# Performance work log

Measured on AMD Instinct MI355X. Metric: run time of the kernel, lower is better.

## Reference

```python
import jax, jax.numpy as jnp
import numpy as np

NUM_HEADS = 8
HEAD_DIM = 128
MAX_RES = 224.0


def rope_embed(feat_shape, dim, max_res=MAX_RES):
    # timm pixel_freq_bands: 2**linspace(0, log2(max_res)-1, dim//4) * pi
    num_bands = dim // 4
    bands = (2.0 ** jnp.linspace(0.0, float(np.log2(max_res)) - 1.0, num_bands)) * jnp.pi
    # pixel coords in [-1, 1] per spatial dim
    coords = [jnp.linspace(-1.0, 1.0, s) for s in feat_shape]
    grid = jnp.stack(jnp.meshgrid(*coords, indexing='ij'), axis=-1)[..., None]  # [H,W,2,1]
    pos = grid * bands  # [H,W,2,num_bands]
    n = int(np.prod(feat_shape))
    sin = jnp.repeat(jnp.sin(pos).reshape(n, -1), 2, axis=-1)  # [n, dim]
    cos = jnp.repeat(jnp.cos(pos).reshape(n, -1), 2, axis=-1)  # [n, dim]
    return sin, cos


def _rot(x):
    # interleaved rotate-half: (x0,x1,x2,x3,...) -> (-x1,x0,-x3,x2,...)
    return jnp.stack([-x[..., 1::2], x[..., ::2]], axis=-1).reshape(x.shape)


def setup_inputs() -> dict:
    key = jax.random.key(0)
    k1, k2, k3, k4 = jax.random.split(key, 4)
    C, E = 1024, 1024
    x = jax.random.normal(k1, (64, C, 16, 16), dtype=jnp.float32)
    qkv_w = jax.random.normal(k2, (3 * E, C), dtype=jnp.float32) * (C ** -0.5)
    qkv_b = jnp.zeros((3 * E,), dtype=jnp.float32)
    proj_w = jax.random.normal(k3, (E, E), dtype=jnp.float32) * (E ** -0.5)
    proj_b = jax.random.normal(k4, (E,), dtype=jnp.float32) * 0.02
    return {"x": x, "qkv_w": qkv_w, "qkv_b": qkv_b, "proj_w": proj_w, "proj_b": proj_b}


def reference(x, qkv_w, qkv_b, proj_w, proj_b):
    B, C, H, W = x.shape
    n = H * W
    scale = HEAD_DIM ** -0.5
    sin_emb, cos_emb = rope_embed((H, W), HEAD_DIM)  # [n, head_dim]

    t = x.reshape(B, C, n).transpose(0, 2, 1)                      # [B, n, C]
    t = jnp.concatenate([t.mean(axis=1, keepdims=True), t], axis=1)  # [B, n+1, C]

    qkv = t @ qkv_w.T + qkv_b                                      # [B, n+1, 3E]
    qkv = qkv.reshape(B, n + 1, 3, NUM_HEADS, HEAD_DIM).transpose(2, 0, 3, 1, 4)
    q, k, v = qkv[0], qkv[1], qkv[2]                               # [B, h, n+1, d]

    def apply_rope(z):
        zc, zs = z[:, :, :1], z[:, :, 1:]
        zs = zs * cos_emb + _rot(zs) * sin_emb
        return jnp.concatenate([zc, zs], axis=2)

    q = apply_rope(q)
    k = apply_rope(k)

    attn = jax.nn.softmax(jnp.einsum('bhqd,bhkd->bhqk', q, k) * scale, axis=-1)
    out = jnp.einsum('bhqk,bhkd->bhqd', attn, v)
    out = out.transpose(0, 2, 1, 3).reshape(B, n + 1, -1)           # [B, n+1, E]
    out = out @ proj_w.T + proj_b
    return out[:, 0]
```

## Files before the change

### kernel.cpp

```cpp
#include <hip/hip_runtime.h>
#include <math.h>

#define PI_F 3.14159265358979323846f
#define KSTEP 0.21959209425992272f

using bf16x8 = __attribute__((ext_vector_type(8))) short;
using f32x4 = __attribute__((ext_vector_type(4))) float;
using u16x8 = __attribute__((ext_vector_type(8))) unsigned short;

static __device__ __forceinline__ float wave_reduce_sum(float v) {
#pragma unroll
  for (int off = 32; off; off >>= 1) v += __shfl_down(v, off);
  return v;
}

static __device__ __forceinline__ unsigned short f2bf(float f) {
  unsigned u = __float_as_uint(f);
  return (unsigned short)((u + 0x7fffu + ((u >> 16) & 1u)) >> 16);
}

static __device__ __forceinline__ float bf2f(unsigned short s) {
  return __uint_as_float(((unsigned)s) << 16);
}

static __device__ __forceinline__ void gload_lds16(const void* g, void* l) {
  __builtin_amdgcn_global_load_lds((const __attribute__((address_space(1))) unsigned int*)g,
                                   (__attribute__((address_space(3))) unsigned int*)l, 16, 0, 0);
}

__global__ __launch_bounds__(256) void prep_kernel(const float* __restrict__ x,
                                                   const float* __restrict__ qkv_w,
                                                   unsigned short* __restrict__ xt,
                                                   float* __restrict__ t_mean,
                                                   unsigned short* __restrict__ wk_bf,
                                                   float2* __restrict__ sc) {
  const int bid = blockIdx.x;
  const int t = threadIdx.x;
  __shared__ float tile[64][33];
  if (bid < 1024) {
    const int ct = bid & 15, b = bid >> 4;
    const int cl = t >> 2, pq = (t & 3) * 8;
    const int pl = t >> 3, cq = (t & 7) * 8;
    float sum = 0.0f;
    const float* xrow = x + ((size_t)(b * 1024 + ct * 64 + cl) * 256) + pq;
    unsigned short* xtb = xt + (size_t)b * 262144 + ct * 64;
    for (int pt = 0; pt < 8; ++pt) {
      const float4 v0 = *reinterpret_cast<const float4*>(xrow + pt * 32);
      const float4 v1 = *reinterpret_cast<const float4*>(xrow + pt * 32 + 4);
      tile[cl][pq + 0] = v0.x; tile[cl][pq + 1] = v0.y; tile[cl][pq + 2] = v0.z; tile[cl][pq + 3] = v0.w;
      tile[cl][pq + 4] = v1.x; tile[cl][pq + 5] = v1.y; tile[cl][pq + 6] = v1.z; tile[cl][pq + 7] = v1.w;
      sum += (v0.x + v0.y) + (v0.z + v0.w) + (v1.x + v1.y) + (v1.z + v1.w);
      __syncthreads();
      u16x8 o;
#pragma unroll
      for (int e = 0; e < 8; ++e) o[e] = f2bf(tile[cq + e][pl]);
      *reinterpret_cast<u16x8*>(xtb + (size_t)(pt * 32 + pl) * 1024 + cq) = o;
      __syncthreads();
    }
    sum += __shfl_xor(sum, 1);
    sum += __shfl_xor(sum, 2);
    if ((t & 3) == 0) t_mean[b * 1024 + ct * 64 + cl] = sum * (1.0f / 256.0f);
  } else if (bid < 2048) {
    const int i = ((bid - 1024) * 256 + t) * 4;
    const float4 v = *reinterpret_cast<const float4*>(qkv_w + 1048576 + i);
    ushort4 r;
    r.x = f2bf(v.x); r.y = f2bf(v.y); r.z = f2bf(v.z); r.w = f2bf(v.w);
    *reinterpret_cast<ushort4*>(wk_bf + i) = r;
  } else {
    const int idx = (bid - 2048) * 256 + t;
    const int m = idx >> 8, j = idx & 255;
    const float band = exp2f((float)(m & 31) * KSTEP) * PI_F;
    const float coord = (m < 32) ? (-1.0f + (2.0f / 15.0f) * (float)(j >> 4))
                                 : (-1.0f + (2.0f / 15.0f) * (float)(j & 15));
    float sn, cs;
    sincosf(coord * band, &sn, &cs);
    sc[idx] = make_float2(sn, cs);
  }
}

__global__ __launch_bounds__(256) void gemm_splitk(
    const float* __restrict__ A, int lda, int aStrideZ,
    const float* __restrict__ B, int ldb, int bStrideZ,
    float* __restrict__ Cp, int ldc, int cStrideZ, int cStrideKc, int KC) {
  const int nt = blockIdx.x, mt = blockIdx.y;
  const int z = blockIdx.z / KC, kc = blockIdx.z % KC;
  const int tid = threadIdx.x;
  A += (size_t)z * aStrideZ + (size_t)mt * 32 * lda + kc * 256;
  B += (size_t)z * bStrideZ + (size_t)nt * 64 * ldb + kc * 256;
  Cp += (size_t)kc * cStrideKc + (size_t)z * cStrideZ + (size_t)mt * 32 * ldc + nt * 64;

  __shared__ float As[32][34];
  __shared__ float Bs[32][68];

  const int tm = tid >> 4;
  const int tn = tid & 15;
  float acc0[4] = {0, 0, 0, 0}, acc1[4] = {0, 0, 0, 0};

  for (int k0 = 0; k0 < 256; k0 += 32) {
    {
      const int m = tid >> 3, kq = tid & 7;
      float4 v = *reinterpret_cast<const float4*>(A + (size_t)m * lda + k0 + kq * 4);
      As[kq * 4 + 0][m] = v.x; As[kq * 4 + 1][m] = v.y;
      As[kq * 4 + 2][m] = v.z; As[kq * 4 + 3][m] = v.w;
    }
#pragma unroll
    for (int r = 0; r < 2; ++r) {
      const int idx = r * 256 + tid;
      const int n = idx >> 3, kq = idx & 7;
      float4 v = *reinterpret_cast<const float4*>(B + (size_t)n * ldb + k0 + kq * 4);
      Bs[kq * 4 + 0][n] = v.x; Bs[kq * 4 + 1][n] = v.y;
      Bs[kq * 4 + 2][n] = v.z; Bs[kq * 4 + 3][n] = v.w;
    }
    __syncthreads();
#pragma unroll
    for (int k = 0; k < 32; ++k) {
      const float a0 = As[k][tm * 2], a1 = As[k][tm * 2 + 1];
      const float4 bb = *reinterpret_cast<const float4*>(&Bs[k][tn * 4]);
      acc0[0] += a0 * bb.x; acc0[1] += a0 * bb.y; acc0[2] += a0 * bb.z; acc0[3] += a0 * bb.w;
      acc1[0] += a1 * bb.x; acc1[1] += a1 * bb.y; acc1[2] += a1 * bb.z; acc1[3] += a1 * bb.w;
    }
    __syncthreads();
  }
  *reinterpret_cast<float4*>(Cp + (size_t)(tm * 2) * ldc + tn * 4) =
      make_float4(acc0[0], acc0[1], acc0[2], acc0[3]);
  *reinterpret_cast<float4*>(Cp + (size_t)(tm * 2 + 1) * ldc + tn * 4) =
      make_float4(acc1[0], acc1[1], acc1[2], acc1[3]);
}

__global__ __launch_bounds__(256) void gemm_proj_splitk(
    const float* __restrict__ Apart, const float* __restrict__ abias,
    const float* __restrict__ B, float* __restrict__ Cp) {
  const int nt = blockIdx.x, mt = blockIdx.y, kc = blockIdx.z;
  const int tid = threadIdx.x;
  B += (size_t)nt * 64 * 1024 + kc * 256;
  Cp += (size_t)kc * 65536 + (size_t)mt * 32 * 1024 + nt * 64;

  __shared__ float As[32][34];
  __shared__ float Bs[32][68];

  const int tm = tid >> 4;
  const int tn = tid & 15;
  float acc0[4] = {0, 0, 0, 0}, acc1[4] = {0, 0, 0, 0};

  for (int k0 = 0; k0 < 256; k0 += 32) {
    {
      const int m = tid >> 3, kq = tid & 7;
      const int kg = kc * 256 + k0 + kq * 4;
      const float* Ab = Apart + (size_t)(mt * 32 + m) * 1024 + kg;
      float4 v = *reinterpret_cast<const float4*>(abias + kg);
#pragma unroll
      for (int r = 0; r < 4; ++r) {
        const float4 p = *reinterpret_cast<const float4*>(Ab + (size_t)r * 65536);
        v.x += p.x; v.y += p.y; v.z += p.z; v.w += p.w;
      }
      As[kq * 4 + 0][m] = v.x; As[kq * 4 + 1][m] = v.y;
      As[kq * 4 + 2][m] = v.z; As[kq * 4 + 3][m] = v.w;
    }
#pragma unroll
    for (int r = 0; r < 2; ++r) {
      const int idx = r * 256 + tid;
      const int n = idx >> 3, kq = idx & 7;
      float4 v = *reinterpret_cast<const float4*>(B + (size_t)n * 1024 + k0 + kq * 4);
      Bs[kq * 4 + 0][n] = v.x; Bs[kq * 4 + 1][n] = v.y;
      Bs[kq * 4 + 2][n] = v.z; Bs[kq * 4 + 3][n] = v.w;
    }
    __syncthreads();
#pragma unroll
    for (int k = 0; k < 32; ++k) {
      const float a0 = As[k][tm * 2], a1 = As[k][tm * 2 + 1];
      const float4 bb = *reinterpret_cast<const float4*>(&Bs[k][tn * 4]);
      acc0[0] += a0 * bb.x; acc0[1] += a0 * bb.y; acc0[2] += a0 * bb.z; acc0[3] += a0 * bb.w;
      acc1[0] += a1 * bb.x; acc1[1] += a1 * bb.y; acc1[2] += a1 * bb.z; acc1[3] += a1 * bb.w;
    }
    __syncthreads();
  }
  *reinterpret_cast<float4*>(Cp + (size_t)(tm * 2) * 1024 + tn * 4) =
      make_float4(acc0[0], acc0[1], acc0[2], acc0[3]);
  *reinterpret_cast<float4*>(Cp + (size_t)(tm * 2 + 1) * 1024 + tn * 4) =
      make_float4(acc1[0], acc1[1], acc1[2], acc1[3]);
}

__global__ __launch_bounds__(256) void reduce4_bias(const float* __restrict__ part,
                                                    const float* __restrict__ bias,
                                                    float* __restrict__ out) {
  const int i = blockIdx.x * 256 + threadIdx.x;
  out[i] = part[i] + part[i + 65536] + part[i + 131072] + part[i + 196608] + bias[i & 1023];
}

__global__ __launch_bounds__(512, 1) void k_scores_mfma(
    const unsigned short* __restrict__ wk, const unsigned short* __restrict__ xt,
    const float* __restrict__ qkv_b, const float* __restrict__ q0p,
    const float2* __restrict__ sc, float* __restrict__ attn) {
  const int l = blockIdx.x;
  const int b = ((l >> 5) << 3) | (l & 7);
  const int mt = (l >> 3) & 3;
  const int tid = threadIdx.x;
  const int w = tid >> 6, lane = tid & 63;
  const int wr = w >> 2, wc = w & 3;

  __shared__ __align__(16) char smem[131072];

  const unsigned short* wkA = wk + (size_t)(mt * 256) * 1024;
  const unsigned short* xtb = xt + (size_t)b * 262144;

  f32x4 acc[8][4] = {};

#define STAGE4(tt, src)                                                          \
  {                                                                              \
    char* base_ = smem + ((tt)&3) * 32768;                                       \
    const int c0_ = (src)*32;                                                    \
    _Pragma("unroll") for (int c = 0; c < 2; ++c) {                              \
      const int rb_ = w * 2 + c;                                                 \
      const int row_ = rb_ * 16 + (lane >> 2);                                   \
      const int sl_ = ((lane & 3) ^ ((row_ >> 1) & 3)) * 8;                      \
      gload_lds16(wkA + (size_t)row_ * 1024 + c0_ + sl_, base_ + rb_ * 1024);    \
      gload_lds16(xtb + (size_t)row_ * 1024 + c0_ + sl_,                         \
                  base_ + 16384 + rb_ * 1024);                                   \
    }                                                                            \
  }

  STAGE4(0, 0);
  STAGE4(1, 1);
  STAGE4(2, 2);

  for (int t = 0; t < 32; ++t) {
    {
      const int tt = t + 3;
      const int src = tt > 31 ? 31 : tt;
      STAGE4(tt, src);
    }
    asm volatile("s_waitcnt vmcnt(12)" ::: "memory");
    __builtin_amdgcn_s_barrier();
    const char* Ab = smem + (t & 3) * 32768;
    const char* Bb = Ab + 16384;
    bf16x8 bfrag[4];
#pragma unroll
    for (int ni = 0; ni < 4; ++ni) {
      const int row = wc * 64 + ni * 16 + (lane & 15);
      bfrag[ni] = *reinterpret_cast<const bf16x8*>(
          Bb + row * 64 + (((lane >> 4) ^ ((row >> 1) & 3)) << 4));
    }
#pragma unroll
    for (int mh = 0; mh < 2; ++mh) {
      bf16x8 af[4];
#pragma unroll
      for (int q = 0; q < 4; ++q) {
        const int row = wr * 128 + (mh * 4 + q) * 16 + (lane & 15);
        af[q] = *reinterpret_cast<const bf16x8*>(
            Ab + row * 64 + (((lane >> 4) ^ ((row >> 1) & 3)) << 4));
      }
      __builtin_amdgcn_s_setprio(1);
#pragma unroll
      for (int q = 0; q < 4; ++q)
#pragma unroll
        for (int ni = 0; ni < 4; ++ni)
          acc[mh * 4 + q][ni] = __builtin_amdgcn_mfma_f32_16x16x32_bf16(
              af[q], bfrag[ni], acc[mh * 4 + q][ni], 0, 0, 0);
      __builtin_amdgcn_s_setprio(0);
    }
    __builtin_amdgcn_s_barrier();
    asm volatile("" ::: "memory");
  }
#undef STAGE4

  asm volatile("s_waitcnt vmcnt(0)" ::: "memory");
  __syncthreads();

  float* q0_lds = reinterpret_cast<float*>(smem);
  float* k0_lds = q0_lds + 256;
  float* Sh = k0_lds + 256;
  float* ps = Sh + 520;
  float* r4 = ps + 4;

  if (tid < 256) {
    const float* qp = q0p + (size_t)b * 2048 + mt * 256 + tid;
    q0_lds[tid] = qkv_b[mt * 256 + tid] + qp[0] + qp[131072] + qp[262144] + qp[393216];
    const float* kp = qp + 1024;
    k0_lds[tid] = qkv_b[1024 + mt * 256 + tid] + kp[0] + kp[131072] + kp[262144] + kp[393216];
  }
  __syncthreads();

  if (tid < 256) {
    float pr = q0_lds[tid] * k0_lds[tid];
    pr = wave_reduce_sum(pr);
    if (lane == 0) ps[tid >> 6] = pr;
  }

  const int colj = lane & 15, rgrp = lane >> 4;
  const float* bk = qkv_b + 1024 + mt * 256 + wr * 128;
  float partial[4] = {0, 0, 0, 0};
#pragma unroll
  for (int mi = 0; mi < 8; ++mi) {
#pragma unroll
    for (int pp = 0; pp < 2; ++pp) {
      const int dd = mi * 16 + rgrp * 4 + pp * 2;
      const int m = dd >> 1;
      const float2 qv = *reinterpret_cast<const float2*>(q0_lds + wr * 128 + dd);
      const float2 bv = *reinterpret_cast<const float2*>(bk + dd);
#pragma unroll
      for (int ni = 0; ni < 4; ++ni) {
        const int j = wc * 64 + ni * 16 + colj;
        const float ke = acc[mi][ni][pp * 2] + bv.x;
        const float ko = acc[mi][ni][pp * 2 + 1] + bv.y;
        const float2 tt = sc[m * 256 + j];
        partial[ni] += tt.y * (ke * qv.x + ko * qv.y) + tt.x * (ke * qv.y - ko * qv.x);
      }
    }
  }
#pragma unroll
  for (int ni = 0; ni < 4; ++ni) {
    partial[ni] += __shfl_xor(partial[ni], 16);
    partial[ni] += __shfl_xor(partial[ni], 32);
  }
  if (lane < 16) {
#pragma unroll
    for (int ni = 0; ni < 4; ++ni)
      Sh[wr * 260 + 1 + wc * 64 + ni * 16 + colj] = partial[ni];
  }
  __syncthreads();
  if (tid == 0) { Sh[0] = ps[0] + ps[1]; Sh[260] = ps[2] + ps[3]; }
  __syncthreads();

  const int hg = tid >> 8, i = tid & 255;
  const float scale = 0.08838834764831845f;
  const float* Sr = Sh + hg * 260;
  const float va = Sr[i] * scale;
  const float vb = (i == 0) ? Sr[256] * scale : -3.0e38f;
  float mx = fmaxf(va, vb);
#pragma unroll
  for (int off = 32; off; off >>= 1) mx = fmaxf(mx, __shfl_xor(mx, off));
  if (lane == 0) r4[hg * 4 + ((tid >> 6) & 3)] = mx;
  __syncthreads();
  mx = fmaxf(fmaxf(r4[hg * 4], r4[hg * 4 + 1]), fmaxf(r4[hg * 4 + 2], r4[hg * 4 + 3]));
  const float ea = expf(va - mx);
  const float eb = (i == 0) ? expf(vb - mx) : 0.0f;
  float sum = ea + eb;
#pragma unroll
  for (int off = 32; off; off >>= 1) sum += __shfl_xor(sum, off);
  __syncthreads();
  if (lane == 0) r4[hg * 4 + ((tid >> 6) & 3)] = sum;
  __syncthreads();
  sum = r4[hg * 4] + r4[hg * 4 + 1] + r4[hg * 4 + 2] + r4[hg * 4 + 3];
  const float inv = 1.0f / sum;
  float* ab = attn + (size_t)(b * 8 + 2 * mt + hg) * 257;
  ab[i] = ea * inv;
  if (i == 0) ab[256] = eb * inv;
}

__global__ __launch_bounds__(256) void u_accum_kernel(const unsigned short* __restrict__ xt,
                                                      const float* __restrict__ t_mean,
                                                      const float* __restrict__ attn,
                                                      float* __restrict__ u) {
  const int ct = blockIdx.x;
  const int b = blockIdx.y;
  const int tid = threadIdx.x;
  __shared__ float aw[2056];
  __shared__ float red[8192];
  for (int i = tid; i < 2056; i += 256) aw[i] = attn[(size_t)(b * 8 + (i & 7)) * 257 + (i >> 3)];
  __syncthreads();
  const int cl = tid & 31, q = tid >> 5;
  const int c = ct * 128 + cl * 4;
  const unsigned short* xr = xt + (size_t)b * 262144 + c;
  float acc[8][4] = {};
  for (int p = q * 32; p < q * 32 + 32; ++p) {
    const ushort4 v = *reinterpret_cast<const ushort4*>(xr + (size_t)p * 1024);
    const float xs[4] = {bf2f(v.x), bf2f(v.y), bf2f(v.z), bf2f(v.w)};
    const float* w8 = &aw[(p + 1) * 8];
#pragma unroll
    for (int hh = 0; hh < 8; ++hh)
#pragma unroll
      for (int e = 0; e < 4; ++e) acc[hh][e] += w8[hh] * xs[e];
  }
#pragma unroll
  for (int hh = 0; hh < 8; ++hh)
#pragma unroll
    for (int e = 0; e < 4; ++e) red[q * 1024 + (cl * 8 + hh) * 4 + e] = acc[hh][e];
  __syncthreads();
#pragma unroll
  for (int r = 0; r < 4; ++r) {
    const int o = tid * 4 + r;
    const int cl2 = o >> 5, hh = (o >> 2) & 7, e = o & 3;
    float s = 0.0f;
#pragma unroll
    for (int qq = 0; qq < 8; ++qq) s += red[qq * 1024 + o];
    const int cc = ct * 128 + cl2 * 4 + e;
    s += aw[hh] * t_mean[b * 1024 + cc];
    u[(size_t)(b * 8 + hh) * 1024 + cc] = s;
  }
}

extern "C" void kernel_launch(void* const* d_in, const int* in_sizes, int n_in,
                              void* d_out, int out_size, void* d_ws, size_t ws_size,
                              hipStream_t stream) {
  const float* x = (const float*)d_in[0];
  const float* qkv_w = (const float*)d_in[1];
  const float* qkv_b = (const float*)d_in[2];
  const float* proj_w = (const float*)d_in[3];
  const float* proj_b = (const float*)d_in[4];
  float* out = (float*)d_out;

  float* ws = (float*)d_ws;
  float* t_mean = ws;
  float* q0k0_part = ws + 65536;
  float* attn = ws + 721408;
  float* u = ws + 852992;
  float* out0_part = ws + 1377280;
  float* out_part = ws + 1639424;
  float2* sc = (float2*)(ws + 1901568);
  unsigned short* wk_bf = (unsigned short*)(ws + 1934336);
  unsigned short* x_t = (unsigned short*)(ws + 2458624);

  prep_kernel<<<2112, 256, 0, stream>>>(x, qkv_w, x_t, t_mean, wk_bf, sc);

  gemm_splitk<<<dim3(32, 2, 4), 256, 0, stream>>>(t_mean, 1024, 0, qkv_w, 1024, 0,
                                                  q0k0_part, 2048, 0, 131072, 4);

  k_scores_mfma<<<256, 512, 0, stream>>>(wk_bf, x_t, qkv_b, q0k0_part, sc, attn);

  u_accum_kernel<<<dim3(8, 64), 256, 0, stream>>>(x_t, t_mean, attn, u);

  gemm_splitk<<<dim3(2, 2, 32), 256, 0, stream>>>(u, 8192, 1024,
                                                  qkv_w + (size_t)2048 * 1024, 1024, 131072,
                                                  out0_part, 1024, 128, 65536, 4);

  gemm_proj_splitk<<<dim3(16, 2, 4), 256, 0, stream>>>(out0_part, qkv_b + 2048, proj_w, out_part);

  reduce4_bias<<<256, 256, 0, stream>>>(out_part, proj_b, out);
}
```

Baseline: 110.1 us.

## Retile scores kernel per head and fuse value projection into u accumulation

The scores kernel now gives each block one head (128 rows) instead of two, halving the accumulators. It switches from a 4-stage to a 3-stage LDS ring with a smaller footprint and raises launch bounds so more blocks can be resident, and the grid doubles to 512 blocks. The u accumulation kernel now also multiplies the per-head u slice by the V weights directly from LDS, writing 8 split-K partials. This removes the separate u buffer and one split-K GEMM launch, and the proj GEMM's A-reduction grows from 4 to 8 partials. The risk is that fp32 weight reads inside the fused kernel are less efficient than the dedicated GEMM.

```diff
diff --git a/kernel.cpp b/kernel.cpp
--- a/kernel.cpp
+++ b/kernel.cpp
@@ -149,7 +149,7 @@
       const float* Ab = Apart + (size_t)(mt * 32 + m) * 1024 + kg;
       float4 v = *reinterpret_cast<const float4*>(abias + kg);
 #pragma unroll
-      for (int r = 0; r < 4; ++r) {
+      for (int r = 0; r < 8; ++r) {
         const float4 p = *reinterpret_cast<const float4*>(Ab + (size_t)r * 65536);
         v.x += p.x; v.y += p.y; v.z += p.z; v.w += p.w;
       }
@@ -187,115 +187,115 @@
   out[i] = part[i] + part[i + 65536] + part[i + 131072] + part[i + 196608] + bias[i & 1023];
 }
 
-__global__ __launch_bounds__(512, 1) void k_scores_mfma(
+__global__ __launch_bounds__(512, 4) void k_scores_mfma(
     const unsigned short* __restrict__ wk, const unsigned short* __restrict__ xt,
     const float* __restrict__ qkv_b, const float* __restrict__ q0p,
     const float2* __restrict__ sc, float* __restrict__ attn) {
   const int l = blockIdx.x;
-  const int b = ((l >> 5) << 3) | (l & 7);
-  const int mt = (l >> 3) & 3;
+  const int b = ((l >> 6) << 3) | (l & 7);
+  const int h = (l >> 3) & 7;
   const int tid = threadIdx.x;
   const int w = tid >> 6, lane = tid & 63;
   const int wr = w >> 2, wc = w & 3;
 
-  __shared__ __align__(16) char smem[131072];
-
-  const unsigned short* wkA = wk + (size_t)(mt * 256) * 1024;
+  __shared__ __align__(16) char smem[73728];
+
+  const unsigned short* wkh = wk + (size_t)h * 131072;
   const unsigned short* xtb = xt + (size_t)b * 262144;
 
-  f32x4 acc[8][4] = {};
-
-#define STAGE4(tt, src)                                                          \
-  {                                                                              \
-    char* base_ = smem + ((tt)&3) * 32768;                                       \
-    const int c0_ = (src)*32;                                                    \
-    _Pragma("unroll") for (int c = 0; c < 2; ++c) {                              \
-      const int rb_ = w * 2 + c;                                                 \
-      const int row_ = rb_ * 16 + (lane >> 2);                                   \
-      const int sl_ = ((lane & 3) ^ ((row_ >> 1) & 3)) * 8;                      \
-      gload_lds16(wkA + (size_t)row_ * 1024 + c0_ + sl_, base_ + rb_ * 1024);    \
-      gload_lds16(xtb + (size_t)row_ * 1024 + c0_ + sl_,                         \
-                  base_ + 16384 + rb_ * 1024);                                   \
-    }                                                                            \
-  }
-
-  STAGE4(0, 0);
-  STAGE4(1, 1);
-  STAGE4(2, 2);
-
+  f32x4 acc[4][4] = {};
+
+#define STAGE6(buf, c0)                                                     \
+  {                                                                         \
+    char* Ab_ = smem + (buf)*24576;                                         \
+    char* Bb_ = Ab_ + 8192;                                                 \
+    {                                                                       \
+      const int row_ = w * 16 + (lane >> 2);                                \
+      const int sl_ = ((lane & 3) ^ ((row_ >> 1) & 3)) * 8;                 \
+      gload_lds16(wkh + (size_t)row_ * 1024 + (c0) + sl_, Ab_ + w * 1024);  \
+    }                                                                       \
+    _Pragma("unroll") for (int i = 0; i < 2; ++i) {                         \
+      const int row_ = w * 32 + i * 16 + (lane >> 2);                       \
+      const int sl_ = ((lane & 3) ^ ((row_ >> 1) & 3)) * 8;                 \
+      gload_lds16(xtb + (size_t)row_ * 1024 + (c0) + sl_,                   \
+                  Bb_ + (w * 2 + i) * 1024);                                \
+    }                                                                       \
+  }
+
+  STAGE6(0, 0);
+  STAGE6(1, 32);
+  int cur = 0, nxt = 2;
   for (int t = 0; t < 32; ++t) {
     {
-      const int tt = t + 3;
-      const int src = tt > 31 ? 31 : tt;
-      STAGE4(tt, src);
-    }
-    asm volatile("s_waitcnt vmcnt(12)" ::: "memory");
+      const int src = (t + 2 > 31) ? 31 : (t + 2);
+      STAGE6(nxt, src * 32);
+    }
+    asm volatile("s_waitcnt vmcnt(6)" ::: "memory");
     __builtin_amdgcn_s_barrier();
-    const char* Ab = smem + (t & 3) * 32768;
-    const char* Bb = Ab + 16384;
-    bf16x8 bfrag[4];
+    const char* Ab = smem + cur * 24576;
+    const char* Bb = Ab + 8192;
+    bf16x8 af[4], bfr[4];
+#pragma unroll
+    for (int mi = 0; mi < 4; ++mi) {
+      const int row = wr * 64 + mi * 16 + (lane & 15);
+      af[mi] = *reinterpret_cast<const bf16x8*>(
+          Ab + row * 64 + (((lane >> 4) ^ ((row >> 1) & 3)) << 4));
+    }
 #pragma unroll
     for (int ni = 0; ni < 4; ++ni) {
       const int row = wc * 64 + ni * 16 + (lane & 15);
-      bfrag[ni] = *reinterpret_cast<const bf16x8*>(
+      bfr[ni] = *reinterpret_cast<const bf16x8*>(
           Bb + row * 64 + (((lane >> 4) ^ ((row >> 1) & 3)) << 4));
     }
-#pragma unroll
-    for (int mh = 0; mh < 2; ++mh) {
-      bf16x8 af[4];
-#pragma unroll
-      for (int q = 0; q < 4; ++q) {
-        const int row = wr * 128 + (mh * 4 + q) * 16 + (lane & 15);
-        af[q] = *reinterpret_cast<const bf16x8*>(
-            Ab + row * 64 + (((lane >> 4) ^ ((row >> 1) & 3)) << 4));
-      }
-      __builtin_amdgcn_s_setprio(1);
-#pragma unroll
-      for (int q = 0; q < 4; ++q)
-#pragma unroll
-        for (int ni = 0; ni < 4; ++ni)
-          acc[mh * 4 + q][ni] = __builtin_amdgcn_mfma_f32_16x16x32_bf16(
-              af[q], bfrag[ni], acc[mh * 4 + q][ni], 0, 0, 0);
-      __builtin_amdgcn_s_setprio(0);
-    }
+    __builtin_amdgcn_s_setprio(1);
+#pragma unroll
+    for (int mi = 0; mi < 4; ++mi)
+#pragma unroll
+      for (int ni = 0; ni < 4; ++ni)
+        acc[mi][ni] =
+            __builtin_amdgcn_mfma_f32_16x16x32_bf16(af[mi], bfr[ni], acc[mi][ni], 0, 0, 0);
+    __builtin_amdgcn_s_setprio(0);
     __builtin_amdgcn_s_barrier();
     asm volatile("" ::: "memory");
-  }
-#undef STAGE4
+    cur = (cur == 2) ? 0 : cur + 1;
+    nxt = (nxt == 2) ? 0 : nxt + 1;
+  }
+#undef STAGE6
 
   asm volatile("s_waitcnt vmcnt(0)" ::: "memory");
   __syncthreads();
 
   float* q0_lds = reinterpret_cast<float*>(smem);
-  float* k0_lds = q0_lds + 256;
-  float* Sh = k0_lds + 256;
-  float* ps = Sh + 520;
-  float* r4 = ps + 4;
-
-  if (tid < 256) {
-    const float* qp = q0p + (size_t)b * 2048 + mt * 256 + tid;
-    q0_lds[tid] = qkv_b[mt * 256 + tid] + qp[0] + qp[131072] + qp[262144] + qp[393216];
+  float* k0_lds = q0_lds + 128;
+  float* red2 = k0_lds + 128;
+  float* ps = red2 + 512;
+  float* r4a = ps + 2;
+  float* r4b = r4a + 4;
+
+  if (tid < 128) {
+    const float* qp = q0p + (size_t)b * 2048 + h * 128 + tid;
+    q0_lds[tid] = qkv_b[h * 128 + tid] + qp[0] + qp[131072] + qp[262144] + qp[393216];
     const float* kp = qp + 1024;
-    k0_lds[tid] = qkv_b[1024 + mt * 256 + tid] + kp[0] + kp[131072] + kp[262144] + kp[393216];
-  }
-  __syncthreads();
-
-  if (tid < 256) {
+    k0_lds[tid] = qkv_b[1024 + h * 128 + tid] + kp[0] + kp[131072] + kp[262144] + kp[393216];
+  }
+  __syncthreads();
+
+  if (tid < 128) {
     float pr = q0_lds[tid] * k0_lds[tid];
     pr = wave_reduce_sum(pr);
-    if (lane == 0) ps[tid >> 6] = pr;
+    if (lane == 0) ps[w] = pr;
   }
 
   const int colj = lane & 15, rgrp = lane >> 4;
-  const float* bk = qkv_b + 1024 + mt * 256 + wr * 128;
+  const float* bk = qkv_b + 1024 + h * 128;
   float partial[4] = {0, 0, 0, 0};
 #pragma unroll
-  for (int mi = 0; mi < 8; ++mi) {
+  for (int mi = 0; mi < 4; ++mi) {
 #pragma unroll
     for (int pp = 0; pp < 2; ++pp) {
-      const int dd = mi * 16 + rgrp * 4 + pp * 2;
+      const int dd = wr * 64 + mi * 16 + rgrp * 4 + pp * 2;
       const int m = dd >> 1;
-      const float2 qv = *reinterpret_cast<const float2*>(q0_lds + wr * 128 + dd);
+      const float2 qv = *reinterpret_cast<const float2*>(q0_lds + dd);
       const float2 bv = *reinterpret_cast<const float2*>(bk + dd);
 #pragma unroll
       for (int ni = 0; ni < 4; ++ni) {
@@ -314,48 +314,53 @@
   }
   if (lane < 16) {
 #pragma unroll
-    for (int ni = 0; ni < 4; ++ni)
-      Sh[wr * 260 + 1 + wc * 64 + ni * 16 + colj] = partial[ni];
-  }
-  __syncthreads();
-  if (tid == 0) { Sh[0] = ps[0] + ps[1]; Sh[260] = ps[2] + ps[3]; }
-  __syncthreads();
-
-  const int hg = tid >> 8, i = tid & 255;
+    for (int ni = 0; ni < 4; ++ni) red2[(wc * 64 + ni * 16 + colj) * 2 + wr] = partial[ni];
+  }
+  __syncthreads();
+
   const float scale = 0.08838834764831845f;
-  const float* Sr = Sh + hg * 260;
-  const float va = Sr[i] * scale;
-  const float vb = (i == 0) ? Sr[256] * scale : -3.0e38f;
+  float va = -3.0e38f, vb = -3.0e38f;
+  if (tid < 256) {
+    va = scale * ((tid == 0) ? (ps[0] + ps[1]) : (red2[(tid - 1) * 2] + red2[(tid - 1) * 2 + 1]));
+    if (tid == 0) vb = scale * (red2[255 * 2] + red2[255 * 2 + 1]);
+  }
   float mx = fmaxf(va, vb);
-#pragma unroll
-  for (int off = 32; off; off >>= 1) mx = fmaxf(mx, __shfl_xor(mx, off));
-  if (lane == 0) r4[hg * 4 + ((tid >> 6) & 3)] = mx;
-  __syncthreads();
-  mx = fmaxf(fmaxf(r4[hg * 4], r4[hg * 4 + 1]), fmaxf(r4[hg * 4 + 2], r4[hg * 4 + 3]));
-  const float ea = expf(va - mx);
-  const float eb = (i == 0) ? expf(vb - mx) : 0.0f;
-  float sum = ea + eb;
-#pragma unroll
-  for (int off = 32; off; off >>= 1) sum += __shfl_xor(sum, off);
-  __syncthreads();
-  if (lane == 0) r4[hg * 4 + ((tid >> 6) & 3)] = sum;
-  __syncthreads();
-  sum = r4[hg * 4] + r4[hg * 4 + 1] + r4[hg * 4 + 2] + r4[hg * 4 + 3];
-  const float inv = 1.0f / sum;
-  float* ab = attn + (size_t)(b * 8 + 2 * mt + hg) * 257;
-  ab[i] = ea * inv;
-  if (i == 0) ab[256] = eb * inv;
-}
-
-__global__ __launch_bounds__(256) void u_accum_kernel(const unsigned short* __restrict__ xt,
-                                                      const float* __restrict__ t_mean,
-                                                      const float* __restrict__ attn,
-                                                      float* __restrict__ u) {
+  if (tid < 256) {
+#pragma unroll
+    for (int off = 32; off; off >>= 1) mx = fmaxf(mx, __shfl_xor(mx, off));
+    if (lane == 0) r4a[w] = mx;
+  }
+  __syncthreads();
+  const float gmx = fmaxf(fmaxf(r4a[0], r4a[1]), fmaxf(r4a[2], r4a[3]));
+  float ea = 0.0f, eb = 0.0f;
+  if (tid < 256) {
+    ea = expf(va - gmx);
+    eb = (tid == 0) ? expf(vb - gmx) : 0.0f;
+    float sm = ea + eb;
+#pragma unroll
+    for (int off = 32; off; off >>= 1) sm += __shfl_xor(sm, off);
+    if (lane == 0) r4b[w] = sm;
+  }
+  __syncthreads();
+  if (tid < 256) {
+    const float inv = 1.0f / (r4b[0] + r4b[1] + r4b[2] + r4b[3]);
+    float* ab = attn + (size_t)(b * 8 + h) * 257;
+    ab[tid] = ea * inv;
+    if (tid == 0) ab[256] = eb * inv;
+  }
+}
+
+__global__ __launch_bounds__(256) void u_out0_kernel(const unsigned short* __restrict__ xt,
+                                                     const float* __restrict__ t_mean,
+                                                     const float* __restrict__ attn,
+                                                     const float* __restrict__ qkv_w,
+                                                     float* __restrict__ out0_part) {
   const int ct = blockIdx.x;
   const int b = blockIdx.y;
   const int tid = threadIdx.x;
   __shared__ float aw[2056];
   __shared__ float red[8192];
+  __shared__ __align__(16) float u_lds[1024];
   for (int i = tid; i < 2056; i += 256) aw[i] = attn[(size_t)(b * 8 + (i & 7)) * 257 + (i >> 3)];
   __syncthreads();
   const int cl = tid & 31, q = tid >> 5;
@@ -383,9 +388,28 @@
     float s = 0.0f;
 #pragma unroll
     for (int qq = 0; qq < 8; ++qq) s += red[qq * 1024 + o];
-    const int cc = ct * 128 + cl2 * 4 + e;
-    s += aw[hh] * t_mean[b * 1024 + cc];
-    u[(size_t)(b * 8 + hh) * 1024 + cc] = s;
+    s += aw[hh] * t_mean[b * 1024 + ct * 128 + cl2 * 4 + e];
+    u_lds[hh * 128 + cl2 * 4 + e] = s;
+  }
+  __syncthreads();
+
+  const int lane7 = tid & 7;
+  float* op = out0_part + (size_t)ct * 65536 + (size_t)b * 1024;
+  for (int s = 0; s < 32; ++s) {
+    const int o = (tid >> 3) + 32 * s;
+    const float* wrow = qkv_w + (size_t)(2048 + o) * 1024 + ct * 128 + lane7 * 16;
+    const float* ur = u_lds + (o >> 7) * 128 + lane7 * 16;
+    float a = 0.0f;
+#pragma unroll
+    for (int i = 0; i < 4; ++i) {
+      const float4 wv = *reinterpret_cast<const float4*>(wrow + i * 4);
+      const float4 uv = *reinterpret_cast<const float4*>(ur + i * 4);
+      a += wv.x * uv.x + wv.y * uv.y + wv.z * uv.z + wv.w * uv.w;
+    }
+    a += __shfl_xor(a, 1);
+    a += __shfl_xor(a, 2);
+    a += __shfl_xor(a, 4);
+    if (lane7 == 0) op[o] = a;
   }
 }
 
@@ -402,26 +426,21 @@
   float* ws = (float*)d_ws;
   float* t_mean = ws;
   float* q0k0_part = ws + 65536;
-  float* attn = ws + 721408;
-  float* u = ws + 852992;
-  float* out0_part = ws + 1377280;
-  float* out_part = ws + 1639424;
-  float2* sc = (float2*)(ws + 1901568);
-  unsigned short* wk_bf = (unsigned short*)(ws + 1934336);
-  unsigned short* x_t = (unsigned short*)(ws + 2458624);
+  float* attn = ws + 589824;
+  float* out0_part = ws + 721408;
+  float* out_part = ws + 1245696;
+  float2* sc = (float2*)(ws + 1507840);
+  unsigned short* wk_bf = (unsigned short*)(ws + 1540608);
+  unsigned short* x_t = (unsigned short*)(ws + 2064896);
 
   prep_kernel<<<2112, 256, 0, stream>>>(x, qkv_w, x_t, t_mean, wk_bf, sc);
 
   gemm_splitk<<<dim3(32, 2, 4), 256, 0, stream>>>(t_mean, 1024, 0, qkv_w, 1024, 0,
                                                   q0k0_part, 2048, 0, 131072, 4);
 
-  k_scores_mfma<<<256, 512, 0, stream>>>(wk_bf, x_t, qkv_b, q0k0_part, sc, attn);
-
-  u_accum_kernel<<<dim3(8, 64), 256, 0, stream>>>(x_t, t_mean, attn, u);
-
-  gemm_splitk<<<dim3(2, 2, 32), 256, 0, stream>>>(u, 8192, 1024,
-                                                  qkv_w + (size_t)2048 * 1024, 1024, 131072,
-                                                  out0_part, 1024, 128, 65536, 4);
+  k_scores_mfma<<<512, 512, 0, stream>>>(wk_bf, x_t, qkv_b, q0k0_part, sc, attn);
+
+  u_out0_kernel<<<dim3(8, 64), 256, 0, stream>>>(x_t, t_mean, attn, qkv_w, out0_part);
 
   gemm_proj_splitk<<<dim3(16, 2, 4), 256, 0, stream>>>(out0_part, qkv_b + 2048, proj_w, out_part);
 
```

Result: slower. 123.6 us (+12.3%).
